# Kernel optimization log

Hardware: AMD Instinct MI355X
Metric: run time of the kernel (lower is better)

Reference implementation:

```python
import jax, jax.numpy as jnp
import numpy as np

B = 262144
NX, NP, T, HDIM = 16, 4, 8, 256
IN_DIM = NX + NP * T   # 48
OUT_DIM = NP * T       # 32
EPS = 1e-5


def _layer_norm(x, g, b):
    m = jnp.mean(x, axis=-1, keepdims=True)
    v = jnp.mean((x - m) ** 2, axis=-1, keepdims=True)
    return (x - m) * jax.lax.rsqrt(v + EPS) * g + b


def setup_inputs() -> dict:
    key = jax.random.key(0)
    ks = jax.random.split(key, 8)
    s = 0.02
    inp = {
        "x": jax.random.normal(ks[0], (B, IN_DIM), jnp.float32),
        "z": jax.random.normal(ks[1], (B, HDIM), jnp.float32),
        # fc_inp
        "W_inp": jax.random.normal(ks[2], (IN_DIM, HDIM), jnp.float32) * s,
        "b_inp": jnp.zeros((HDIM,), jnp.float32),
        "g_ln_inp": jnp.ones((HDIM,), jnp.float32),
        "b_ln_inp": jnp.zeros((HDIM,), jnp.float32),
        # fcdeq1 / lndeq1
        "W1": jax.random.normal(ks[3], (HDIM, HDIM), jnp.float32) * s,
        "b1": jnp.zeros((HDIM,), jnp.float32),
        "g_ln1": jnp.ones((HDIM,), jnp.float32),
        "b_ln1": jnp.zeros((HDIM,), jnp.float32),
        # fcdeq2 / lndeq2
        "W2": jax.random.normal(ks[4], (HDIM, HDIM), jnp.float32) * s,
        "b2": jnp.zeros((HDIM,), jnp.float32),
        "g_ln2": jnp.ones((HDIM,), jnp.float32),
        "b_ln2": jnp.zeros((HDIM,), jnp.float32),
        # lndeq3
        "g_ln3": jnp.ones((HDIM,), jnp.float32),
        "b_ln3": jnp.zeros((HDIM,), jnp.float32),
        # fc_out
        "W_out": jax.random.normal(ks[5], (HDIM, OUT_DIM), jnp.float32) * s,
        "b_out": jnp.zeros((OUT_DIM,), jnp.float32),
    }
    return inp


def reference(x, z, W_inp, b_inp, g_ln_inp, b_ln_inp,
              W1, b1, g_ln1, b_ln1, W2, b2, g_ln2, b_ln2,
              g_ln3, b_ln3, W_out, b_out):
    # xinp = ln_inp(fc_inp(x))
    xinp = _layer_norm(x @ W_inp + b_inp, g_ln_inp, b_ln_inp)
    # deq_layer(xinp, z)
    z1 = _layer_norm(jax.nn.relu(z @ W1 + b1), g_ln1, b_ln1)
    inner = _layer_norm(xinp + z1 @ W2 + b2, g_ln2, b_ln2)
    z_out = _layer_norm(jax.nn.relu(z1 + inner), g_ln3, b_ln3)
    # fc_out + reshape to (B, T, np)
    dx_ref = (z_out @ W_out + b_out).reshape(-1, T, NP)
    return (dx_ref, z_out)
```

## Files before the change

kernel.cpp:

```cpp
#include <hip/hip_runtime.h>
#include <hip/hip_bf16.h>

typedef float  f32x4  __attribute__((ext_vector_type(4)));
typedef float  f32x16 __attribute__((ext_vector_type(16)));
typedef short  s16x8  __attribute__((ext_vector_type(8)));
typedef unsigned int u32;

__device__ __forceinline__ short f2bf(float f) {
    union { float f; u32 u; } c; c.f = f;
    return (short)((c.u + 0x8000u) >> 16);
}
__device__ __forceinline__ float bf2f(u32 v) {
    union { u32 u; float f; } c; c.u = v << 16; return c.f;
}
__device__ __forceinline__ u32 cvtpk(float lo, float hi) {
    u32 r;
    asm("v_cvt_pk_bf16_f32 %0, %1, %2" : "=v"(r) : "v"(lo), "v"(hi));
    return r;
}
__device__ __forceinline__ s16x8 cvt8(float4 f0, float4 f1) {
    union { s16x8 v; u32 w[4]; } u;
    u.w[0] = cvtpk(f0.x, f0.y); u.w[1] = cvtpk(f0.z, f0.w);
    u.w[2] = cvtpk(f1.x, f1.y); u.w[3] = cvtpk(f1.z, f1.w);
    return u.v;
}
__device__ __forceinline__ s16x8 cvt8v(f32x4 a, f32x4 b) {
    union { s16x8 v; u32 w[4]; } u;
    u.w[0] = cvtpk(a[0], a[1]); u.w[1] = cvtpk(a[2], a[3]);
    u.w[2] = cvtpk(b[0], b[1]); u.w[3] = cvtpk(b[2], b[3]);
    return u.v;
}
__device__ __forceinline__ void gload16(const void* g, void* l) {
    __builtin_amdgcn_global_load_lds((const __attribute__((address_space(1))) u32*)g,
                                     (__attribute__((address_space(3))) u32*)l, 16, 0, 0);
}

#define MFMA32(a, b, c) __builtin_amdgcn_mfma_f32_32x32x16_bf16((a), (b), (c), 0, 0, 0)
#define MFMA16(a, b, c) __builtin_amdgcn_mfma_f32_16x16x32_bf16((a), (b), (c), 0, 0, 0)

__global__ void pack_w(const float* __restrict__ W, short* __restrict__ out,
                       int Kreal, int N, int nbTot, int total) {
    int tid = blockIdx.x * 256 + threadIdx.x;
    if (tid >= total) return;
    int j  = tid & 7;
    int l  = (tid >> 3) & 63;
    int blk = tid >> 9;
    int nb = blk % nbTot, ks = blk / nbTot;
    int k = ks * 32 + (l >> 4) * 8 + j;
    int n = nb * 16 + (l & 15);
    out[tid] = (k < Kreal) ? f2bf(W[(long)k * N + n]) : (short)0;
}

__global__ void pack_w32(const float* __restrict__ W, short* __restrict__ out,
                         int Kreal, int N, int nbTot, int total) {
    int tid = blockIdx.x * 256 + threadIdx.x;
    if (tid >= total) return;
    int j  = tid & 7;
    int l  = (tid >> 3) & 63;
    int blk = tid >> 9;
    int nb = blk % nbTot, ks = blk / nbTot;
    int k = ks * 16 + (l >> 5) * 8 + j;
    int n = nb * 32 + (l & 31);
    out[tid] = (k < Kreal) ? f2bf(W[(long)k * N + n]) : (short)0;
}

__device__ __forceinline__ void initC(f32x16& a, const float* p, int base, int hi) {
#pragma unroll
    for (int q = 0; q < 4; ++q) {
        float4 v = *(const float4*)(p + base + q * 8 + hi * 4);
        a[q * 4 + 0] = v.x; a[q * 4 + 1] = v.y; a[q * 4 + 2] = v.z; a[q * 4 + 3] = v.w;
    }
}
__device__ __forceinline__ void addC(f32x16& a, const float* p, int base, int hi) {
#pragma unroll
    for (int q = 0; q < 4; ++q) {
        float4 v = *(const float4*)(p + base + q * 8 + hi * 4);
        a[q * 4 + 0] += v.x; a[q * 4 + 1] += v.y; a[q * 4 + 2] += v.z; a[q * 4 + 3] += v.w;
    }
}

__device__ __forceinline__ void ln32(f32x16& a0, f32x16& a1,
                                     const float* __restrict__ g, const float* __restrict__ bl,
                                     float2* red, int lane, int b, int hi, int w, int fb) {
    float s = 0.f, q = 0.f;
#pragma unroll
    for (int i = 0; i < 16; ++i) {
        s += a0[i] + a1[i];
        q += a0[i] * a0[i] + a1[i] * a1[i];
    }
    s += __shfl_xor(s, 32); q += __shfl_xor(q, 32);
    if (lane < 32) red[b * 4 + w] = make_float2(s, q);
    __syncthreads();
    float2 p0 = red[b * 4 + 0], p1 = red[b * 4 + 1];
    float2 p2 = red[b * 4 + 2], p3 = red[b * 4 + 3];
    float S = (p0.x + p1.x) + (p2.x + p3.x);
    float Q = (p0.y + p1.y) + (p2.y + p3.y);
    float mean = S * (1.f / 256.f);
    float var  = fmaxf(Q * (1.f / 256.f) - mean * mean, 0.f);
    float rstd = rsqrtf(var + 1e-5f);
#pragma unroll
    for (int nb = 0; nb < 2; ++nb) {
        f32x16& a = nb ? a1 : a0;
#pragma unroll
        for (int qd = 0; qd < 4; ++qd) {
            float4 gv = *(const float4*)(g  + fb + nb * 32 + qd * 8 + hi * 4);
            float4 bv = *(const float4*)(bl + fb + nb * 32 + qd * 8 + hi * 4);
            a[qd * 4 + 0] = (a[qd * 4 + 0] - mean) * rstd * gv.x + bv.x;
            a[qd * 4 + 1] = (a[qd * 4 + 1] - mean) * rstd * gv.y + bv.y;
            a[qd * 4 + 2] = (a[qd * 4 + 2] - mean) * rstd * gv.z + bv.z;
            a[qd * 4 + 3] = (a[qd * 4 + 3] - mean) * rstd * gv.w + bv.w;
        }
    }
}

__global__ __launch_bounds__(256, 4) void deq_main(
    const float* __restrict__ x, const float* __restrict__ z,
    const float* __restrict__ b_inp, const float* __restrict__ g_lni, const float* __restrict__ b_lni,
    const float* __restrict__ b1, const float* __restrict__ g_ln1, const float* __restrict__ b_ln1,
    const float* __restrict__ b2, const float* __restrict__ g_ln2, const float* __restrict__ b_ln2,
    const float* __restrict__ g_ln3, const float* __restrict__ b_ln3,
    const float* __restrict__ b_out,
    const s16x8* __restrict__ Wp1, const s16x8* __restrict__ Wp2,
    const s16x8* __restrict__ WpI, const s16x8* __restrict__ WpO,
    float* __restrict__ out_dx, float* __restrict__ out_z)
{
    __shared__ __align__(16) char smem[36 * 1024];
    short*  T_sh = (short*)smem;
    float2* red  = (float2*)(smem + 32 * 1024);

    const int tid  = threadIdx.x;
    const int w    = tid >> 6;
    const int lane = tid & 63;
    const int b    = lane & 31;
    const int hi   = lane >> 5;
    const int fb   = w * 64;
    const int fbn  = w * 2;
    const int r = lane & 15, kg = lane >> 4;
    const long r0 = (long)blockIdx.x * 32;
    const int swzb = (b & 7) << 4;

#pragma unroll
    for (int i = 0; i < 8; ++i) {
        int row = w * 8 + i;
        const char* gp = (const char*)(z + (r0 + row) * 256) + ((lane * 16) ^ ((row & 7) << 4));
        gload16(gp, smem + row * 1024);
    }

    float4 xv0, xv1, xv2, xv3, xv4, xv5;
    {
        const float* xr = x + (r0 + b) * 48 + hi * 8;
        xv0 = ((const float4*)(xr))[0];      xv1 = ((const float4*)(xr + 4))[0];
        xv2 = ((const float4*)(xr + 16))[0]; xv3 = ((const float4*)(xr + 20))[0];
        xv4 = ((const float4*)(xr + 32))[0]; xv5 = ((const float4*)(xr + 36))[0];
    }
    __syncthreads();

    f32x16 acc0, acc1;

    initC(acc0, b1, fb, hi);
    initC(acc1, b1, fb + 32, hi);
    {
        const char* zrow = (const char*)smem + b * 1024;
        s16x8 c0 = Wp1[(fbn + 0) * 64 + lane];
        s16x8 c1 = Wp1[(fbn + 1) * 64 + lane];
#pragma unroll
        for (int ks = 0; ks < 16; ++ks) {
            s16x8 n0, n1;
            if (ks < 15) {
                n0 = Wp1[((ks + 1) * 8 + fbn + 0) * 64 + lane];
                n1 = Wp1[((ks + 1) * 8 + fbn + 1) * 64 + lane];
            }
            const int c = ks * 64 + hi * 32;
            f32x4 p0 = *(const f32x4*)(zrow + ((c) ^ swzb));
            f32x4 p1 = *(const f32x4*)(zrow + ((c + 16) ^ swzb));
            s16x8 a = cvt8v(p0, p1);
            acc0 = MFMA32(c0, a, acc0);
            acc1 = MFMA32(c1, a, acc1);
            c0 = n0; c1 = n1;
        }
    }

#pragma unroll
    for (int i = 0; i < 16; ++i) { acc0[i] = fmaxf(acc0[i], 0.f); acc1[i] = fmaxf(acc1[i], 0.f); }
    ln32(acc0, acc1, g_ln1, b_ln1, red + 0 * 128, lane, b, hi, w, fb);

    u32 z1p[2][8];
#pragma unroll
    for (int nb = 0; nb < 2; ++nb) {
        f32x16& a = nb ? acc1 : acc0;
#pragma unroll
        for (int qd = 0; qd < 4; ++qd) {
            z1p[nb][qd * 2 + 0] = cvtpk(a[qd * 4 + 0], a[qd * 4 + 1]);
            z1p[nb][qd * 2 + 1] = cvtpk(a[qd * 4 + 2], a[qd * 4 + 3]);
        }
    }
#pragma unroll
    for (int nb = 0; nb < 2; ++nb)
#pragma unroll
        for (int qd = 0; qd < 4; ++qd) {
            int fbyte = (fb + nb * 32 + qd * 8 + hi * 4) * 2;
            *(uint2*)((char*)T_sh + b * 512 + (fbyte ^ swzb)) =
                make_uint2(z1p[nb][qd * 2], z1p[nb][qd * 2 + 1]);
        }

    initC(acc0, b_inp, fb, hi);
    initC(acc1, b_inp, fb + 32, hi);
    {
        s16x8 a0 = cvt8(xv0, xv1);
        s16x8 a1 = cvt8(xv2, xv3);
        s16x8 a2 = cvt8(xv4, xv5);
        acc0 = MFMA32(WpI[(0 * 8 + fbn + 0) * 64 + lane], a0, acc0);
        acc1 = MFMA32(WpI[(0 * 8 + fbn + 1) * 64 + lane], a0, acc1);
        acc0 = MFMA32(WpI[(1 * 8 + fbn + 0) * 64 + lane], a1, acc0);
        acc1 = MFMA32(WpI[(1 * 8 + fbn + 1) * 64 + lane], a1, acc1);
        acc0 = MFMA32(WpI[(2 * 8 + fbn + 0) * 64 + lane], a2, acc0);
        acc1 = MFMA32(WpI[(2 * 8 + fbn + 1) * 64 + lane], a2, acc1);
    }
    ln32(acc0, acc1, g_lni, b_lni, red + 1 * 128, lane, b, hi, w, fb);

    addC(acc0, b2, fb, hi);
    addC(acc1, b2, fb + 32, hi);

    {
        const char* zr = (const char*)T_sh + b * 512;
        s16x8 c0 = Wp2[(fbn + 0) * 64 + lane];
        s16x8 c1 = Wp2[(fbn + 1) * 64 + lane];
#pragma unroll
        for (int ks = 0; ks < 16; ++ks) {
            s16x8 n0, n1;
            if (ks < 15) {
                n0 = Wp2[((ks + 1) * 8 + fbn + 0) * 64 + lane];
                n1 = Wp2[((ks + 1) * 8 + fbn + 1) * 64 + lane];
            }
            s16x8 az = *(const s16x8*)(zr + ((ks * 32 + hi * 16) ^ swzb));
            acc0 = MFMA32(c0, az, acc0);
            acc1 = MFMA32(c1, az, acc1);
            c0 = n0; c1 = n1;
        }
    }
    ln32(acc0, acc1, g_ln2, b_ln2, red + 2 * 128, lane, b, hi, w, fb);

#pragma unroll
    for (int nb = 0; nb < 2; ++nb) {
        f32x16& a = nb ? acc1 : acc0;
#pragma unroll
        for (int qd = 0; qd < 4; ++qd) {
            a[qd * 4 + 0] = fmaxf(a[qd * 4 + 0] + bf2f(z1p[nb][qd * 2] & 0xffffu), 0.f);
            a[qd * 4 + 1] = fmaxf(a[qd * 4 + 1] + bf2f(z1p[nb][qd * 2] >> 16), 0.f);
            a[qd * 4 + 2] = fmaxf(a[qd * 4 + 2] + bf2f(z1p[nb][qd * 2 + 1] & 0xffffu), 0.f);
            a[qd * 4 + 3] = fmaxf(a[qd * 4 + 3] + bf2f(z1p[nb][qd * 2 + 1] >> 16), 0.f);
        }
    }
    ln32(acc0, acc1, g_ln3, b_ln3, red + 3 * 128, lane, b, hi, w, fb);

#pragma unroll
    for (int nb = 0; nb < 2; ++nb) {
        f32x16& a = nb ? acc1 : acc0;
#pragma unroll
        for (int qd = 0; qd < 4; ++qd) {
            u32 w0 = cvtpk(a[qd * 4 + 0], a[qd * 4 + 1]);
            u32 w1 = cvtpk(a[qd * 4 + 2], a[qd * 4 + 3]);
            int fbyte = (fb + nb * 32 + qd * 8 + hi * 4) * 2;
            *(uint2*)((char*)T_sh + b * 512 + (fbyte ^ swzb)) = make_uint2(w0, w1);
        }
    }
    __syncthreads();

    {
        const int mi = w & 1, nbo = w >> 1;
        float bb = b_out[nbo * 16 + r];
        f32x4 ao = (f32x4){bb, bb, bb, bb};
#pragma unroll
        for (int ks = 0; ks < 8; ++ks) {
            int R = mi * 16 + r;
            int off = R * 512 + ((ks * 64 + kg * 16) ^ ((R & 7) << 4));
            s16x8 a0 = *(const s16x8*)((const char*)T_sh + off);
            s16x8 bw = WpO[(ks * 2 + nbo) * 64 + lane];
            ao = MFMA16(a0, bw, ao);
        }
#pragma unroll
        for (int j = 0; j < 4; ++j)
            out_dx[(r0 + mi * 16 + kg * 4 + j) * 32 + nbo * 16 + r] = ao[j];
    }

    {
        float* zo = out_z + r0 * 256;
#pragma unroll
        for (int it = 0; it < 4; ++it) {
            int row = w * 8 + it * 2 + (lane >> 5);
            int addr = row * 512 + (((lane & 31) * 16) ^ ((row & 7) << 4));
            int4 wd = *(const int4*)((const char*)T_sh + addr);
            float4 o0, o1;
            o0.x = bf2f((u32)wd.x & 0xffffu); o0.y = bf2f((u32)wd.x >> 16);
            o0.z = bf2f((u32)wd.y & 0xffffu); o0.w = bf2f((u32)wd.y >> 16);
            o1.x = bf2f((u32)wd.z & 0xffffu); o1.y = bf2f((u32)wd.z >> 16);
            o1.z = bf2f((u32)wd.w & 0xffffu); o1.w = bf2f((u32)wd.w >> 16);
            int e = row * 256 + (lane & 31) * 8;
            *(float4*)(zo + e) = o0;
            *(float4*)(zo + e + 4) = o1;
        }
    }
}

extern "C" void kernel_launch(void* const* d_in, const int* in_sizes, int n_in,
                              void* d_out, int out_size, void* d_ws, size_t ws_size,
                              hipStream_t stream) {
    const float* x      = (const float*)d_in[0];
    const float* z      = (const float*)d_in[1];
    const float* W_inp  = (const float*)d_in[2];
    const float* b_inp  = (const float*)d_in[3];
    const float* g_lni  = (const float*)d_in[4];
    const float* b_lni  = (const float*)d_in[5];
    const float* W1     = (const float*)d_in[6];
    const float* b1     = (const float*)d_in[7];
    const float* g_ln1  = (const float*)d_in[8];
    const float* b_ln1  = (const float*)d_in[9];
    const float* W2     = (const float*)d_in[10];
    const float* b2     = (const float*)d_in[11];
    const float* g_ln2  = (const float*)d_in[12];
    const float* b_ln2  = (const float*)d_in[13];
    const float* g_ln3  = (const float*)d_in[14];
    const float* b_ln3  = (const float*)d_in[15];
    const float* W_out  = (const float*)d_in[16];
    const float* b_out  = (const float*)d_in[17];

    short* Wp1 = (short*)d_ws;
    short* Wp2 = Wp1 + 65536;
    short* WpI = Wp2 + 65536;
    short* WpO = WpI + 12288;

    pack_w32<<<256, 256, 0, stream>>>(W1,    Wp1, 256, 256, 8, 65536);
    pack_w32<<<256, 256, 0, stream>>>(W2,    Wp2, 256, 256, 8, 65536);
    pack_w32<<< 48, 256, 0, stream>>>(W_inp, WpI,  48, 256, 8, 12288);
    pack_w  <<< 32, 256, 0, stream>>>(W_out, WpO, 256,  32, 2,  8192);

    const long B = 262144;
    float* out_dx = (float*)d_out;
    float* out_z  = out_dx + B * 32;
    deq_main<<<B / 32, 256, 0, stream>>>(x, z, b_inp, g_lni, b_lni,
                                         b1, g_ln1, b_ln1, b2, g_ln2, b_ln2,
                                         g_ln3, b_ln3, b_out,
                                         (const s16x8*)Wp1, (const s16x8*)Wp2,
                                         (const s16x8*)WpI, (const s16x8*)WpO,
                                         out_dx, out_z);
}
```

Baseline: 283.5 us.

## Hoist input-projection MFMAs before the z barrier, deepen weight prefetch, pad z rows

Moves the x @ W_inp MFMA computation ahead of the barrier that waits for the async z tile load, so it overlaps with that load. The weight-fragment prefetch in both 256x256 GEMM loops is deepened from one to two k-steps ahead. The XOR swizzle on the fp32 z tile is replaced by padding each row to 1040 bytes. Together these aim to hide global-load latency and simplify LDS addressing, at the cost of more live registers (a second pair of 16-wide accumulators plus extra prefetch fragments) and slightly more shared memory, which could reduce occupancy under the 256x4 launch bounds.

```diff
diff --git a/kernel.cpp b/kernel.cpp
--- a/kernel.cpp
+++ b/kernel.cpp
@@ -37,6 +37,7 @@
 
 #define MFMA32(a, b, c) __builtin_amdgcn_mfma_f32_32x32x16_bf16((a), (b), (c), 0, 0, 0)
 #define MFMA16(a, b, c) __builtin_amdgcn_mfma_f32_16x16x32_bf16((a), (b), (c), 0, 0, 0)
+#define ZS 1040
 
 __global__ void pack_w(const float* __restrict__ W, short* __restrict__ out,
                        int Kreal, int N, int nbTot, int total) {
@@ -124,9 +125,9 @@
     const s16x8* __restrict__ WpI, const s16x8* __restrict__ WpO,
     float* __restrict__ out_dx, float* __restrict__ out_z)
 {
-    __shared__ __align__(16) char smem[36 * 1024];
+    __shared__ __align__(16) char smem[32 * ZS + 4096];
     short*  T_sh = (short*)smem;
-    float2* red  = (float2*)(smem + 32 * 1024);
+    float2* red  = (float2*)(smem + 32 * ZS);
 
     const int tid  = threadIdx.x;
     const int w    = tid >> 6;
@@ -142,41 +143,56 @@
 #pragma unroll
     for (int i = 0; i < 8; ++i) {
         int row = w * 8 + i;
-        const char* gp = (const char*)(z + (r0 + row) * 256) + ((lane * 16) ^ ((row & 7) << 4));
-        gload16(gp, smem + row * 1024);
-    }
-
-    float4 xv0, xv1, xv2, xv3, xv4, xv5;
+        const char* gp = (const char*)(z + (r0 + row) * 256) + lane * 16;
+        gload16(gp, smem + row * ZS);
+    }
+
+    f32x16 xacc0, xacc1;
+    initC(xacc0, b_inp, fb, hi);
+    initC(xacc1, b_inp, fb + 32, hi);
     {
         const float* xr = x + (r0 + b) * 48 + hi * 8;
-        xv0 = ((const float4*)(xr))[0];      xv1 = ((const float4*)(xr + 4))[0];
-        xv2 = ((const float4*)(xr + 16))[0]; xv3 = ((const float4*)(xr + 20))[0];
-        xv4 = ((const float4*)(xr + 32))[0]; xv5 = ((const float4*)(xr + 36))[0];
-    }
-    __syncthreads();
+        float4 xv0 = ((const float4*)(xr))[0],      xv1 = ((const float4*)(xr + 4))[0];
+        float4 xv2 = ((const float4*)(xr + 16))[0], xv3 = ((const float4*)(xr + 20))[0];
+        float4 xv4 = ((const float4*)(xr + 32))[0], xv5 = ((const float4*)(xr + 36))[0];
+        s16x8 a0 = cvt8(xv0, xv1);
+        s16x8 a1 = cvt8(xv2, xv3);
+        s16x8 a2 = cvt8(xv4, xv5);
+        xacc0 = MFMA32(WpI[(0 * 8 + fbn + 0) * 64 + lane], a0, xacc0);
+        xacc1 = MFMA32(WpI[(0 * 8 + fbn + 1) * 64 + lane], a0, xacc1);
+        xacc0 = MFMA32(WpI[(1 * 8 + fbn + 0) * 64 + lane], a1, xacc0);
+        xacc1 = MFMA32(WpI[(1 * 8 + fbn + 1) * 64 + lane], a1, xacc1);
+        xacc0 = MFMA32(WpI[(2 * 8 + fbn + 0) * 64 + lane], a2, xacc0);
+        xacc1 = MFMA32(WpI[(2 * 8 + fbn + 1) * 64 + lane], a2, xacc1);
+    }
+
+    s16x8 c0 = Wp1[(fbn + 0) * 64 + lane];
+    s16x8 c1 = Wp1[(fbn + 1) * 64 + lane];
+    s16x8 d0 = Wp1[(8 + fbn + 0) * 64 + lane];
+    s16x8 d1 = Wp1[(8 + fbn + 1) * 64 + lane];
 
     f32x16 acc0, acc1;
-
     initC(acc0, b1, fb, hi);
     initC(acc1, b1, fb + 32, hi);
-    {
-        const char* zrow = (const char*)smem + b * 1024;
-        s16x8 c0 = Wp1[(fbn + 0) * 64 + lane];
-        s16x8 c1 = Wp1[(fbn + 1) * 64 + lane];
+
+    __syncthreads();
+
+    {
+        const char* zrow = (const char*)smem + b * ZS;
 #pragma unroll
         for (int ks = 0; ks < 16; ++ks) {
-            s16x8 n0, n1;
-            if (ks < 15) {
-                n0 = Wp1[((ks + 1) * 8 + fbn + 0) * 64 + lane];
-                n1 = Wp1[((ks + 1) * 8 + fbn + 1) * 64 + lane];
+            s16x8 e0, e1;
+            if (ks < 14) {
+                e0 = Wp1[((ks + 2) * 8 + fbn + 0) * 64 + lane];
+                e1 = Wp1[((ks + 2) * 8 + fbn + 1) * 64 + lane];
             }
             const int c = ks * 64 + hi * 32;
-            f32x4 p0 = *(const f32x4*)(zrow + ((c) ^ swzb));
-            f32x4 p1 = *(const f32x4*)(zrow + ((c + 16) ^ swzb));
+            f32x4 p0 = *(const f32x4*)(zrow + c);
+            f32x4 p1 = *(const f32x4*)(zrow + c + 16);
             s16x8 a = cvt8v(p0, p1);
             acc0 = MFMA32(c0, a, acc0);
             acc1 = MFMA32(c1, a, acc1);
-            c0 = n0; c1 = n1;
+            c0 = d0; c1 = d1; d0 = e0; d1 = e1;
         }
     }
 
@@ -203,46 +219,36 @@
                 make_uint2(z1p[nb][qd * 2], z1p[nb][qd * 2 + 1]);
         }
 
-    initC(acc0, b_inp, fb, hi);
-    initC(acc1, b_inp, fb + 32, hi);
-    {
-        s16x8 a0 = cvt8(xv0, xv1);
-        s16x8 a1 = cvt8(xv2, xv3);
-        s16x8 a2 = cvt8(xv4, xv5);
-        acc0 = MFMA32(WpI[(0 * 8 + fbn + 0) * 64 + lane], a0, acc0);
-        acc1 = MFMA32(WpI[(0 * 8 + fbn + 1) * 64 + lane], a0, acc1);
-        acc0 = MFMA32(WpI[(1 * 8 + fbn + 0) * 64 + lane], a1, acc0);
-        acc1 = MFMA32(WpI[(1 * 8 + fbn + 1) * 64 + lane], a1, acc1);
-        acc0 = MFMA32(WpI[(2 * 8 + fbn + 0) * 64 + lane], a2, acc0);
-        acc1 = MFMA32(WpI[(2 * 8 + fbn + 1) * 64 + lane], a2, acc1);
-    }
-    ln32(acc0, acc1, g_lni, b_lni, red + 1 * 128, lane, b, hi, w, fb);
-
-    addC(acc0, b2, fb, hi);
-    addC(acc1, b2, fb + 32, hi);
+    c0 = Wp2[(fbn + 0) * 64 + lane];
+    c1 = Wp2[(fbn + 1) * 64 + lane];
+    d0 = Wp2[(8 + fbn + 0) * 64 + lane];
+    d1 = Wp2[(8 + fbn + 1) * 64 + lane];
+
+    ln32(xacc0, xacc1, g_lni, b_lni, red + 1 * 128, lane, b, hi, w, fb);
+
+    addC(xacc0, b2, fb, hi);
+    addC(xacc1, b2, fb + 32, hi);
 
     {
         const char* zr = (const char*)T_sh + b * 512;
-        s16x8 c0 = Wp2[(fbn + 0) * 64 + lane];
-        s16x8 c1 = Wp2[(fbn + 1) * 64 + lane];
 #pragma unroll
         for (int ks = 0; ks < 16; ++ks) {
-            s16x8 n0, n1;
-            if (ks < 15) {
-                n0 = Wp2[((ks + 1) * 8 + fbn + 0) * 64 + lane];
-                n1 = Wp2[((ks + 1) * 8 + fbn + 1) * 64 + lane];
+            s16x8 e0, e1;
+            if (ks < 14) {
+                e0 = Wp2[((ks + 2) * 8 + fbn + 0) * 64 + lane];
+                e1 = Wp2[((ks + 2) * 8 + fbn + 1) * 64 + lane];
             }
             s16x8 az = *(const s16x8*)(zr + ((ks * 32 + hi * 16) ^ swzb));
-            acc0 = MFMA32(c0, az, acc0);
-            acc1 = MFMA32(c1, az, acc1);
-            c0 = n0; c1 = n1;
-        }
-    }
-    ln32(acc0, acc1, g_ln2, b_ln2, red + 2 * 128, lane, b, hi, w, fb);
+            xacc0 = MFMA32(c0, az, xacc0);
+            xacc1 = MFMA32(c1, az, xacc1);
+            c0 = d0; c1 = d1; d0 = e0; d1 = e1;
+        }
+    }
+    ln32(xacc0, xacc1, g_ln2, b_ln2, red + 2 * 128, lane, b, hi, w, fb);
 
 #pragma unroll
     for (int nb = 0; nb < 2; ++nb) {
-        f32x16& a = nb ? acc1 : acc0;
+        f32x16& a = nb ? xacc1 : xacc0;
 #pragma unroll
         for (int qd = 0; qd < 4; ++qd) {
             a[qd * 4 + 0] = fmaxf(a[qd * 4 + 0] + bf2f(z1p[nb][qd * 2] & 0xffffu), 0.f);
@@ -251,11 +257,11 @@
             a[qd * 4 + 3] = fmaxf(a[qd * 4 + 3] + bf2f(z1p[nb][qd * 2 + 1] >> 16), 0.f);
         }
     }
-    ln32(acc0, acc1, g_ln3, b_ln3, red + 3 * 128, lane, b, hi, w, fb);
+    ln32(xacc0, xacc1, g_ln3, b_ln3, red + 3 * 128, lane, b, hi, w, fb);
 
 #pragma unroll
     for (int nb = 0; nb < 2; ++nb) {
-        f32x16& a = nb ? acc1 : acc0;
+        f32x16& a = nb ? xacc1 : xacc0;
 #pragma unroll
         for (int qd = 0; qd < 4; ++qd) {
             u32 w0 = cvtpk(a[qd * 4 + 0], a[qd * 4 + 1]);
```

Measured after the change: 335.9 us. 18.5% more time.

## Process 64 rows per block, reusing each weight fragment across two row tiles

Applied to the files above, without the earlier changes.

Each block now handles 64 batch rows instead of 32, and every loaded weight fragment feeds two MFMAs, one per 32-row half. This halves weight traffic per row. The z tile is converted to bf16 on the way into LDS with ordinary loads instead of async fp32 global_load_lds. The z1 residual is kept in LDS rather than in packed registers, and the two layernorm reduction buffers alternate between stages. In exchange the kernel holds four accumulators, which raises register pressure and may lower occupancy under the 4-blocks launch bound, and the z load is no longer asynchronous.

```diff
diff --git a/kernel.cpp b/kernel.cpp
--- a/kernel.cpp
+++ b/kernel.cpp
@@ -23,16 +23,6 @@
     u.w[0] = cvtpk(f0.x, f0.y); u.w[1] = cvtpk(f0.z, f0.w);
     u.w[2] = cvtpk(f1.x, f1.y); u.w[3] = cvtpk(f1.z, f1.w);
     return u.v;
-}
-__device__ __forceinline__ s16x8 cvt8v(f32x4 a, f32x4 b) {
-    union { s16x8 v; u32 w[4]; } u;
-    u.w[0] = cvtpk(a[0], a[1]); u.w[1] = cvtpk(a[2], a[3]);
-    u.w[2] = cvtpk(b[0], b[1]); u.w[3] = cvtpk(b[2], b[3]);
-    return u.v;
-}
-__device__ __forceinline__ void gload16(const void* g, void* l) {
-    __builtin_amdgcn_global_load_lds((const __attribute__((address_space(1))) u32*)g,
-                                     (__attribute__((address_space(3))) u32*)l, 16, 0, 0);
 }
 
 #define MFMA32(a, b, c) __builtin_amdgcn_mfma_f32_32x32x16_bf16((a), (b), (c), 0, 0, 0)
@@ -79,36 +69,47 @@
     }
 }
 
-__device__ __forceinline__ void ln32(f32x16& a0, f32x16& a1,
+__device__ __forceinline__ void ln64(f32x16& a00, f32x16& a01, f32x16& a10, f32x16& a11,
                                      const float* __restrict__ g, const float* __restrict__ bl,
                                      float2* red, int lane, int b, int hi, int w, int fb) {
-    float s = 0.f, q = 0.f;
+    float sA = 0.f, qA = 0.f, sB = 0.f, qB = 0.f;
 #pragma unroll
     for (int i = 0; i < 16; ++i) {
-        s += a0[i] + a1[i];
-        q += a0[i] * a0[i] + a1[i] * a1[i];
-    }
-    s += __shfl_xor(s, 32); q += __shfl_xor(q, 32);
-    if (lane < 32) red[b * 4 + w] = make_float2(s, q);
+        sA += a00[i] + a01[i]; qA += a00[i] * a00[i] + a01[i] * a01[i];
+        sB += a10[i] + a11[i]; qB += a10[i] * a10[i] + a11[i] * a11[i];
+    }
+    sA += __shfl_xor(sA, 32); qA += __shfl_xor(qA, 32);
+    sB += __shfl_xor(sB, 32); qB += __shfl_xor(qB, 32);
+    if (lane < 32) {
+        red[b * 4 + w] = make_float2(sA, qA);
+        red[(b + 32) * 4 + w] = make_float2(sB, qB);
+    }
     __syncthreads();
-    float2 p0 = red[b * 4 + 0], p1 = red[b * 4 + 1];
-    float2 p2 = red[b * 4 + 2], p3 = red[b * 4 + 3];
-    float S = (p0.x + p1.x) + (p2.x + p3.x);
-    float Q = (p0.y + p1.y) + (p2.y + p3.y);
-    float mean = S * (1.f / 256.f);
-    float var  = fmaxf(Q * (1.f / 256.f) - mean * mean, 0.f);
-    float rstd = rsqrtf(var + 1e-5f);
+    float2 a0 = red[b * 4 + 0], a1 = red[b * 4 + 1], a2 = red[b * 4 + 2], a3 = red[b * 4 + 3];
+    float2 c0 = red[(b + 32) * 4 + 0], c1 = red[(b + 32) * 4 + 1];
+    float2 c2 = red[(b + 32) * 4 + 2], c3 = red[(b + 32) * 4 + 3];
+    float SA = (a0.x + a1.x) + (a2.x + a3.x), QA = (a0.y + a1.y) + (a2.y + a3.y);
+    float SB = (c0.x + c1.x) + (c2.x + c3.x), QB = (c0.y + c1.y) + (c2.y + c3.y);
+    float mA = SA * (1.f / 256.f);
+    float rA = rsqrtf(fmaxf(QA * (1.f / 256.f) - mA * mA, 0.f) + 1e-5f);
+    float mB = SB * (1.f / 256.f);
+    float rB = rsqrtf(fmaxf(QB * (1.f / 256.f) - mB * mB, 0.f) + 1e-5f);
 #pragma unroll
     for (int nb = 0; nb < 2; ++nb) {
-        f32x16& a = nb ? a1 : a0;
+        f32x16& xA = nb ? a01 : a00;
+        f32x16& xB = nb ? a11 : a10;
 #pragma unroll
         for (int qd = 0; qd < 4; ++qd) {
             float4 gv = *(const float4*)(g  + fb + nb * 32 + qd * 8 + hi * 4);
             float4 bv = *(const float4*)(bl + fb + nb * 32 + qd * 8 + hi * 4);
-            a[qd * 4 + 0] = (a[qd * 4 + 0] - mean) * rstd * gv.x + bv.x;
-            a[qd * 4 + 1] = (a[qd * 4 + 1] - mean) * rstd * gv.y + bv.y;
-            a[qd * 4 + 2] = (a[qd * 4 + 2] - mean) * rstd * gv.z + bv.z;
-            a[qd * 4 + 3] = (a[qd * 4 + 3] - mean) * rstd * gv.w + bv.w;
+            xA[qd * 4 + 0] = (xA[qd * 4 + 0] - mA) * rA * gv.x + bv.x;
+            xA[qd * 4 + 1] = (xA[qd * 4 + 1] - mA) * rA * gv.y + bv.y;
+            xA[qd * 4 + 2] = (xA[qd * 4 + 2] - mA) * rA * gv.z + bv.z;
+            xA[qd * 4 + 3] = (xA[qd * 4 + 3] - mA) * rA * gv.w + bv.w;
+            xB[qd * 4 + 0] = (xB[qd * 4 + 0] - mB) * rB * gv.x + bv.x;
+            xB[qd * 4 + 1] = (xB[qd * 4 + 1] - mB) * rB * gv.y + bv.y;
+            xB[qd * 4 + 2] = (xB[qd * 4 + 2] - mB) * rB * gv.z + bv.z;
+            xB[qd * 4 + 3] = (xB[qd * 4 + 3] - mB) * rB * gv.w + bv.w;
         }
     }
 }
@@ -124,9 +125,8 @@
     const s16x8* __restrict__ WpI, const s16x8* __restrict__ WpO,
     float* __restrict__ out_dx, float* __restrict__ out_z)
 {
-    __shared__ __align__(16) char smem[36 * 1024];
-    short*  T_sh = (short*)smem;
-    float2* red  = (float2*)(smem + 32 * 1024);
+    __shared__ __align__(16) short Z_sh[64 * 256];
+    __shared__ float2 red0[64 * 4], red1[64 * 4];
 
     const int tid  = threadIdx.x;
     const int w    = tid >> 6;
@@ -136,31 +136,30 @@
     const int fb   = w * 64;
     const int fbn  = w * 2;
     const int r = lane & 15, kg = lane >> 4;
-    const long r0 = (long)blockIdx.x * 32;
-    const int swzb = (b & 7) << 4;
+    const long r0 = (long)blockIdx.x * 64;
+    const int swzb = b << 4;
 
 #pragma unroll
     for (int i = 0; i < 8; ++i) {
-        int row = w * 8 + i;
-        const char* gp = (const char*)(z + (r0 + row) * 256) + ((lane * 16) ^ ((row & 7) << 4));
-        gload16(gp, smem + row * 1024);
-    }
-
-    float4 xv0, xv1, xv2, xv3, xv4, xv5;
-    {
-        const float* xr = x + (r0 + b) * 48 + hi * 8;
-        xv0 = ((const float4*)(xr))[0];      xv1 = ((const float4*)(xr + 4))[0];
-        xv2 = ((const float4*)(xr + 16))[0]; xv3 = ((const float4*)(xr + 20))[0];
-        xv4 = ((const float4*)(xr + 32))[0]; xv5 = ((const float4*)(xr + 36))[0];
+        int c = i * 256 + tid;
+        int row = c >> 5, ch = c & 31;
+        const float4* gp = (const float4*)(z + (r0 + row) * 256 + ch * 8);
+        float4 f0 = gp[0], f1 = gp[1];
+        union { int4 v; u32 u[4]; } pk;
+        pk.u[0] = cvtpk(f0.x, f0.y); pk.u[1] = cvtpk(f0.z, f0.w);
+        pk.u[2] = cvtpk(f1.x, f1.y); pk.u[3] = cvtpk(f1.z, f1.w);
+        *(int4*)((char*)Z_sh + row * 512 + ((ch * 16) ^ ((row & 31) << 4))) = pk.v;
     }
     __syncthreads();
 
-    f32x16 acc0, acc1;
-
-    initC(acc0, b1, fb, hi);
-    initC(acc1, b1, fb + 32, hi);
-    {
-        const char* zrow = (const char*)smem + b * 1024;
+    f32x16 acc00, acc01, acc10, acc11;
+
+    initC(acc00, b1, fb, hi);
+    initC(acc01, b1, fb + 32, hi);
+    acc10 = acc00; acc11 = acc01;
+    {
+        const char* zr0 = (const char*)Z_sh + b * 512;
+        const char* zr1 = zr0 + 32 * 512;
         s16x8 c0 = Wp1[(fbn + 0) * 64 + lane];
         s16x8 c1 = Wp1[(fbn + 1) * 64 + lane];
 #pragma unroll
@@ -170,59 +169,70 @@
                 n0 = Wp1[((ks + 1) * 8 + fbn + 0) * 64 + lane];
                 n1 = Wp1[((ks + 1) * 8 + fbn + 1) * 64 + lane];
             }
-            const int c = ks * 64 + hi * 32;
-            f32x4 p0 = *(const f32x4*)(zrow + ((c) ^ swzb));
-            f32x4 p1 = *(const f32x4*)(zrow + ((c + 16) ^ swzb));
-            s16x8 a = cvt8v(p0, p1);
-            acc0 = MFMA32(c0, a, acc0);
-            acc1 = MFMA32(c1, a, acc1);
+            int off = (ks * 32 + hi * 16) ^ swzb;
+            s16x8 aA = *(const s16x8*)(zr0 + off);
+            s16x8 aB = *(const s16x8*)(zr1 + off);
+            acc00 = MFMA32(c0, aA, acc00);
+            acc10 = MFMA32(c0, aB, acc10);
+            acc01 = MFMA32(c1, aA, acc01);
+            acc11 = MFMA32(c1, aB, acc11);
             c0 = n0; c1 = n1;
         }
     }
 
 #pragma unroll
-    for (int i = 0; i < 16; ++i) { acc0[i] = fmaxf(acc0[i], 0.f); acc1[i] = fmaxf(acc1[i], 0.f); }
-    ln32(acc0, acc1, g_ln1, b_ln1, red + 0 * 128, lane, b, hi, w, fb);
-
-    u32 z1p[2][8];
-#pragma unroll
-    for (int nb = 0; nb < 2; ++nb) {
-        f32x16& a = nb ? acc1 : acc0;
-#pragma unroll
-        for (int qd = 0; qd < 4; ++qd) {
-            z1p[nb][qd * 2 + 0] = cvtpk(a[qd * 4 + 0], a[qd * 4 + 1]);
-            z1p[nb][qd * 2 + 1] = cvtpk(a[qd * 4 + 2], a[qd * 4 + 3]);
-        }
-    }
-#pragma unroll
-    for (int nb = 0; nb < 2; ++nb)
-#pragma unroll
-        for (int qd = 0; qd < 4; ++qd) {
-            int fbyte = (fb + nb * 32 + qd * 8 + hi * 4) * 2;
-            *(uint2*)((char*)T_sh + b * 512 + (fbyte ^ swzb)) =
-                make_uint2(z1p[nb][qd * 2], z1p[nb][qd * 2 + 1]);
-        }
-
-    initC(acc0, b_inp, fb, hi);
-    initC(acc1, b_inp, fb + 32, hi);
-    {
-        s16x8 a0 = cvt8(xv0, xv1);
-        s16x8 a1 = cvt8(xv2, xv3);
-        s16x8 a2 = cvt8(xv4, xv5);
-        acc0 = MFMA32(WpI[(0 * 8 + fbn + 0) * 64 + lane], a0, acc0);
-        acc1 = MFMA32(WpI[(0 * 8 + fbn + 1) * 64 + lane], a0, acc1);
-        acc0 = MFMA32(WpI[(1 * 8 + fbn + 0) * 64 + lane], a1, acc0);
-        acc1 = MFMA32(WpI[(1 * 8 + fbn + 1) * 64 + lane], a1, acc1);
-        acc0 = MFMA32(WpI[(2 * 8 + fbn + 0) * 64 + lane], a2, acc0);
-        acc1 = MFMA32(WpI[(2 * 8 + fbn + 1) * 64 + lane], a2, acc1);
-    }
-    ln32(acc0, acc1, g_lni, b_lni, red + 1 * 128, lane, b, hi, w, fb);
-
-    addC(acc0, b2, fb, hi);
-    addC(acc1, b2, fb + 32, hi);
-
-    {
-        const char* zr = (const char*)T_sh + b * 512;
+    for (int i = 0; i < 16; ++i) {
+        acc00[i] = fmaxf(acc00[i], 0.f); acc01[i] = fmaxf(acc01[i], 0.f);
+        acc10[i] = fmaxf(acc10[i], 0.f); acc11[i] = fmaxf(acc11[i], 0.f);
+    }
+    ln64(acc00, acc01, acc10, acc11, g_ln1, b_ln1, red0, lane, b, hi, w, fb);
+
+#pragma unroll
+    for (int hf = 0; hf < 2; ++hf) {
+        int row = b + hf * 32;
+#pragma unroll
+        for (int nb = 0; nb < 2; ++nb) {
+            f32x16& a = hf ? (nb ? acc11 : acc10) : (nb ? acc01 : acc00);
+#pragma unroll
+            for (int qd = 0; qd < 4; ++qd) {
+                u32 w0 = cvtpk(a[qd * 4 + 0], a[qd * 4 + 1]);
+                u32 w1 = cvtpk(a[qd * 4 + 2], a[qd * 4 + 3]);
+                int fbyte = (fb + nb * 32 + qd * 8 + hi * 4) * 2;
+                *(uint2*)((char*)Z_sh + row * 512 + (fbyte ^ swzb)) = make_uint2(w0, w1);
+            }
+        }
+    }
+
+    initC(acc00, b_inp, fb, hi);
+    initC(acc01, b_inp, fb + 32, hi);
+    acc10 = acc00; acc11 = acc01;
+    {
+        const float* xr0 = x + (r0 + b) * 48 + hi * 8;
+        const float* xr1 = x + (r0 + 32 + b) * 48 + hi * 8;
+#pragma unroll
+        for (int ks = 0; ks < 3; ++ks) {
+            float4 fA0 = ((const float4*)(xr0 + ks * 16))[0];
+            float4 fA1 = ((const float4*)(xr0 + ks * 16 + 4))[0];
+            float4 fB0 = ((const float4*)(xr1 + ks * 16))[0];
+            float4 fB1 = ((const float4*)(xr1 + ks * 16 + 4))[0];
+            s16x8 aA = cvt8(fA0, fA1);
+            s16x8 aB = cvt8(fB0, fB1);
+            s16x8 w0 = WpI[(ks * 8 + fbn + 0) * 64 + lane];
+            s16x8 w1 = WpI[(ks * 8 + fbn + 1) * 64 + lane];
+            acc00 = MFMA32(w0, aA, acc00);
+            acc10 = MFMA32(w0, aB, acc10);
+            acc01 = MFMA32(w1, aA, acc01);
+            acc11 = MFMA32(w1, aB, acc11);
+        }
+    }
+    ln64(acc00, acc01, acc10, acc11, g_lni, b_lni, red1, lane, b, hi, w, fb);
+
+    addC(acc00, b2, fb, hi);      addC(acc01, b2, fb + 32, hi);
+    addC(acc10, b2, fb, hi);      addC(acc11, b2, fb + 32, hi);
+
+    {
+        const char* zr0 = (const char*)Z_sh + b * 512;
+        const char* zr1 = zr0 + 32 * 512;
         s16x8 c0 = Wp2[(fbn + 0) * 64 + lane];
         s16x8 c1 = Wp2[(fbn + 1) * 64 + lane];
 #pragma unroll
@@ -232,64 +242,85 @@
                 n0 = Wp2[((ks + 1) * 8 + fbn + 0) * 64 + lane];
                 n1 = Wp2[((ks + 1) * 8 + fbn + 1) * 64 + lane];
             }
-            s16x8 az = *(const s16x8*)(zr + ((ks * 32 + hi * 16) ^ swzb));
-            acc0 = MFMA32(c0, az, acc0);
-            acc1 = MFMA32(c1, az, acc1);
+            int off = (ks * 32 + hi * 16) ^ swzb;
+            s16x8 aA = *(const s16x8*)(zr0 + off);
+            s16x8 aB = *(const s16x8*)(zr1 + off);
+            acc00 = MFMA32(c0, aA, acc00);
+            acc10 = MFMA32(c0, aB, acc10);
+            acc01 = MFMA32(c1, aA, acc01);
+            acc11 = MFMA32(c1, aB, acc11);
             c0 = n0; c1 = n1;
         }
     }
-    ln32(acc0, acc1, g_ln2, b_ln2, red + 2 * 128, lane, b, hi, w, fb);
-
-#pragma unroll
-    for (int nb = 0; nb < 2; ++nb) {
-        f32x16& a = nb ? acc1 : acc0;
-#pragma unroll
-        for (int qd = 0; qd < 4; ++qd) {
-            a[qd * 4 + 0] = fmaxf(a[qd * 4 + 0] + bf2f(z1p[nb][qd * 2] & 0xffffu), 0.f);
-            a[qd * 4 + 1] = fmaxf(a[qd * 4 + 1] + bf2f(z1p[nb][qd * 2] >> 16), 0.f);
-            a[qd * 4 + 2] = fmaxf(a[qd * 4 + 2] + bf2f(z1p[nb][qd * 2 + 1] & 0xffffu), 0.f);
-            a[qd * 4 + 3] = fmaxf(a[qd * 4 + 3] + bf2f(z1p[nb][qd * 2 + 1] >> 16), 0.f);
-        }
-    }
-    ln32(acc0, acc1, g_ln3, b_ln3, red + 3 * 128, lane, b, hi, w, fb);
-
-#pragma unroll
-    for (int nb = 0; nb < 2; ++nb) {
-        f32x16& a = nb ? acc1 : acc0;
-#pragma unroll
-        for (int qd = 0; qd < 4; ++qd) {
-            u32 w0 = cvtpk(a[qd * 4 + 0], a[qd * 4 + 1]);
-            u32 w1 = cvtpk(a[qd * 4 + 2], a[qd * 4 + 3]);
-            int fbyte = (fb + nb * 32 + qd * 8 + hi * 4) * 2;
-            *(uint2*)((char*)T_sh + b * 512 + (fbyte ^ swzb)) = make_uint2(w0, w1);
+    ln64(acc00, acc01, acc10, acc11, g_ln2, b_ln2, red0, lane, b, hi, w, fb);
+
+#pragma unroll
+    for (int hf = 0; hf < 2; ++hf) {
+        int row = b + hf * 32;
+#pragma unroll
+        for (int nb = 0; nb < 2; ++nb) {
+            f32x16& a = hf ? (nb ? acc11 : acc10) : (nb ? acc01 : acc00);
+#pragma unroll
+            for (int qd = 0; qd < 4; ++qd) {
+                int fbyte = (fb + nb * 32 + qd * 8 + hi * 4) * 2;
+                uint2 v = *(const uint2*)((const char*)Z_sh + row * 512 + (fbyte ^ swzb));
+                a[qd * 4 + 0] = fmaxf(a[qd * 4 + 0] + bf2f(v.x & 0xffffu), 0.f);
+                a[qd * 4 + 1] = fmaxf(a[qd * 4 + 1] + bf2f(v.x >> 16), 0.f);
+                a[qd * 4 + 2] = fmaxf(a[qd * 4 + 2] + bf2f(v.y & 0xffffu), 0.f);
+                a[qd * 4 + 3] = fmaxf(a[qd * 4 + 3] + bf2f(v.y >> 16), 0.f);
+            }
+        }
+    }
+    ln64(acc00, acc01, acc10, acc11, g_ln3, b_ln3, red1, lane, b, hi, w, fb);
+
+#pragma unroll
+    for (int hf = 0; hf < 2; ++hf) {
+        int row = b + hf * 32;
+#pragma unroll
+        for (int nb = 0; nb < 2; ++nb) {
+            f32x16& a = hf ? (nb ? acc11 : acc10) : (nb ? acc01 : acc00);
+#pragma unroll
+            for (int qd = 0; qd < 4; ++qd) {
+                u32 w0 = cvtpk(a[qd * 4 + 0], a[qd * 4 + 1]);
+                u32 w1 = cvtpk(a[qd * 4 + 2], a[qd * 4 + 3]);
+                int fbyte = (fb + nb * 32 + qd * 8 + hi * 4) * 2;
+                *(uint2*)((char*)Z_sh + row * 512 + (fbyte ^ swzb)) = make_uint2(w0, w1);
+            }
         }
     }
     __syncthreads();
 
     {
-        const int mi = w & 1, nbo = w >> 1;
-        float bb = b_out[nbo * 16 + r];
-        f32x4 ao = (f32x4){bb, bb, bb, bb};
+        f32x4 ao[2];
+#pragma unroll
+        for (int nbo = 0; nbo < 2; ++nbo) {
+            float bb = b_out[nbo * 16 + r];
+            ao[nbo] = (f32x4){bb, bb, bb, bb};
+        }
+        const int R = w * 16 + r;
+        const int swzR = (R & 31) << 4;
 #pragma unroll
         for (int ks = 0; ks < 8; ++ks) {
-            int R = mi * 16 + r;
-            int off = R * 512 + ((ks * 64 + kg * 16) ^ ((R & 7) << 4));
-            s16x8 a0 = *(const s16x8*)((const char*)T_sh + off);
-            s16x8 bw = WpO[(ks * 2 + nbo) * 64 + lane];
-            ao = MFMA16(a0, bw, ao);
-        }
-#pragma unroll
-        for (int j = 0; j < 4; ++j)
-            out_dx[(r0 + mi * 16 + kg * 4 + j) * 32 + nbo * 16 + r] = ao[j];
+            int off = R * 512 + ((ks * 64 + kg * 16) ^ swzR);
+            s16x8 a0 = *(const s16x8*)((const char*)Z_sh + off);
+#pragma unroll
+            for (int nbo = 0; nbo < 2; ++nbo)
+                ao[nbo] = MFMA16(a0, WpO[(ks * 2 + nbo) * 64 + lane], ao[nbo]);
+        }
+#pragma unroll
+        for (int nbo = 0; nbo < 2; ++nbo)
+#pragma unroll
+            for (int j = 0; j < 4; ++j)
+                out_dx[(r0 + w * 16 + kg * 4 + j) * 32 + nbo * 16 + r] = ao[nbo][j];
     }
 
     {
         float* zo = out_z + r0 * 256;
 #pragma unroll
-        for (int it = 0; it < 4; ++it) {
-            int row = w * 8 + it * 2 + (lane >> 5);
-            int addr = row * 512 + (((lane & 31) * 16) ^ ((row & 7) << 4));
-            int4 wd = *(const int4*)((const char*)T_sh + addr);
+        for (int it = 0; it < 8; ++it) {
+            int row = w * 16 + it * 2 + (lane >> 5);
+            int addr = row * 512 + (((lane & 31) * 16) ^ ((row & 31) << 4));
+            int4 wd = *(const int4*)((const char*)Z_sh + addr);
             float4 o0, o1;
             o0.x = bf2f((u32)wd.x & 0xffffu); o0.y = bf2f((u32)wd.x >> 16);
             o0.z = bf2f((u32)wd.y & 0xffffu); o0.w = bf2f((u32)wd.y >> 16);
@@ -337,7 +368,7 @@
     const long B = 262144;
     float* out_dx = (float*)d_out;
     float* out_z  = out_dx + B * 32;
-    deq_main<<<B / 32, 256, 0, stream>>>(x, z, b_inp, g_lni, b_lni,
+    deq_main<<<B / 64, 256, 0, stream>>>(x, z, b_inp, g_lni, b_lni,
                                          b1, g_ln1, b_ln1, b2, g_ln2, b_ln2,
                                          g_ln3, b_ln3, b_out,
                                          (const s16x8*)Wp1, (const s16x8*)Wp2,
```

New measurement: 246.5 us, median of 2. 13.0% less time.
